# Optimization experiments

Measured on AMD Instinct MI355X. Metric: run time of the kernel, lower is better.

The kernel has to match this reference:

```python
import jax, jax.numpy as jnp
import numpy as np


def setup_inputs() -> dict:
    key = jax.random.key(0)
    kx, ky = jax.random.split(key)
    x = jax.random.normal(kx, (16, 4096, 3), dtype=jnp.float32)
    y = jax.random.normal(ky, (16, 4096, 3), dtype=jnp.float32)
    return {"x": x, "y": y}


def reference(x, y):
    # avoiding the O(b*N*M*d) difference tensor of the naive expansion.
    x2 = jnp.sum(x * x, axis=-1)                  # (b, N)
    y2 = jnp.sum(y * y, axis=-1)                  # (b, M)
    xy = jnp.einsum('bnd,bmd->bnm', x, y)         # (b, N, M)
    dist = x2[:, :, None] + y2[:, None, :] - 2.0 * xy
    min_d = jnp.min(dist, axis=2)                 # top-1 smallest over M -> (b, N)
    chamfer = jnp.sum(min_d, axis=1) / x.shape[1] # (b,)
    return jnp.sum(chamfer)
```

## Files before the change

### kernel.cpp

```cpp
#include <hip/hip_runtime.h>


constexpr int NPTS   = 4096;
constexpr int NBATCH = 16;
constexpr int BLOCK  = 256;
constexpr int XPT    = 8;
constexpr int XCHUNK = BLOCK * XPT;
constexpr int NXC    = NPTS / XCHUNK;
constexpr int NYC    = 64;
constexpr int YT     = NPTS / NYC;


__global__ __launch_bounds__(BLOCK, 8) void chamfer_part_kernel(
    const float* __restrict__ x, const float* __restrict__ y,
    float* __restrict__ ws)
{
    __shared__ float4 sy[YT];

    const int b      = blockIdx.x / (NXC * NYC);
    const int xchunk = (blockIdx.x / NYC) % NXC;
    const int ychunk = blockIdx.x % NYC;

    if (threadIdx.x < YT) {
        const float* yp = y + ((size_t)b * NPTS + ychunk * YT + threadIdx.x) * 3;
        const float y0 = yp[0], y1 = yp[1], y2 = yp[2];
        sy[threadIdx.x] = make_float4(2.0f * y0, 2.0f * y1, 2.0f * y2,
                                      fmaf(y2, y2, fmaf(y1, y1, y0 * y0)));
    }

    const int xbase = xchunk * XCHUNK + threadIdx.x * XPT;
    const float4* xp4 = (const float4*)(x + ((size_t)b * NPTS + xbase) * 3);
    float xf[24];
    #pragma unroll
    for (int q = 0; q < 6; ++q) {
        const float4 a = xp4[q];
        xf[4 * q + 0] = a.x; xf[4 * q + 1] = a.y;
        xf[4 * q + 2] = a.z; xf[4 * q + 3] = a.w;
    }

    __syncthreads();

    float m[XPT];
    #pragma unroll
    for (int i = 0; i < XPT; ++i) m[i] = 3.4e38f;

    #pragma unroll 1
    for (int j = 0; j < YT; j += 2) {
        const float4 Y0 = sy[j];
        const float4 Y1 = sy[j + 1];
        #pragma unroll
        for (int i = 0; i < XPT; ++i) {
            const float t0 = fmaf(-xf[3 * i + 0], Y0.x,
                             fmaf(-xf[3 * i + 1], Y0.y,
                             fmaf(-xf[3 * i + 2], Y0.z, Y0.w)));
            const float t1 = fmaf(-xf[3 * i + 0], Y1.x,
                             fmaf(-xf[3 * i + 1], Y1.y,
                             fmaf(-xf[3 * i + 2], Y1.z, Y1.w)));
            m[i] = fminf(fminf(t0, t1), m[i]);
        }
    }

    float* wp = ws + ((size_t)b * NYC + ychunk) * NPTS + xbase;
    #pragma unroll
    for (int i = 0; i < XPT; i += 4) {
        float4 o;
        float* oc = (float*)&o;
        #pragma unroll
        for (int k = 0; k < 4; ++k) {
            const int p = i + k;
            const float x2 = fmaf(xf[3 * p + 2], xf[3 * p + 2],
                             fmaf(xf[3 * p + 1], xf[3 * p + 1],
                                  xf[3 * p + 0] * xf[3 * p + 0]));
            oc[k] = fmaxf(x2 + m[p], 0.0f);
        }
        ((float4*)wp)[i / 4] = o;
    }
}


__global__ __launch_bounds__(BLOCK) void chamfer_reduce_kernel(
    const float* __restrict__ ws, float* __restrict__ out)
{
    __shared__ float swsum[BLOCK / 64];
    const int idx = blockIdx.x * BLOCK + threadIdx.x;
    const int b   = idx / NPTS;
    const int xp  = idx % NPTS;

    const float* p = ws + (size_t)b * NYC * NPTS + xp;
    float mn = 3.4e38f;
    #pragma unroll 8
    for (int yc = 0; yc < NYC; ++yc)
        mn = fminf(mn, p[(size_t)yc * NPTS]);

    float s = mn;
    for (int off = 32; off > 0; off >>= 1)
        s += __shfl_down(s, off, 64);
    const int wave = threadIdx.x >> 6;
    if ((threadIdx.x & 63) == 0) swsum[wave] = s;
    __syncthreads();
    if (threadIdx.x == 0) {
        float t = 0.f;
        #pragma unroll
        for (int w = 0; w < BLOCK / 64; ++w) t += swsum[w];
        atomicAdd(out, t * (1.0f / NPTS));
    }
}


__global__ __launch_bounds__(BLOCK) void chamfer_min_atomic_kernel(
    const float* __restrict__ x, const float* __restrict__ y,
    unsigned int* __restrict__ ws_min)
{
    constexpr int YTILE = 256;
    constexpr int FNYC  = NPTS / YTILE;
    __shared__ float4 sy[YTILE];

    const int b      = blockIdx.x / (NXC * FNYC);
    const int xchunk = (blockIdx.x / FNYC) % NXC;
    const int ychunk = blockIdx.x % FNYC;

    {
        const float* yp = y + ((size_t)b * NPTS + ychunk * YTILE + threadIdx.x) * 3;
        const float y0 = yp[0], y1 = yp[1], y2 = yp[2];
        sy[threadIdx.x] = make_float4(2.0f * y0, 2.0f * y1, 2.0f * y2,
                                      fmaf(y2, y2, fmaf(y1, y1, y0 * y0)));
    }

    const int xbase = xchunk * XCHUNK + threadIdx.x * XPT;
    const float4* xp4 = (const float4*)(x + ((size_t)b * NPTS + xbase) * 3);
    float xf[24];
    #pragma unroll
    for (int q = 0; q < 6; ++q) {
        const float4 a = xp4[q];
        xf[4 * q + 0] = a.x; xf[4 * q + 1] = a.y;
        xf[4 * q + 2] = a.z; xf[4 * q + 3] = a.w;
    }

    __syncthreads();

    float m[XPT];
    #pragma unroll
    for (int i = 0; i < XPT; ++i) m[i] = 3.4e38f;

    #pragma unroll 1
    for (int j = 0; j < YTILE; j += 2) {
        const float4 Y0 = sy[j];
        const float4 Y1 = sy[j + 1];
        #pragma unroll
        for (int i = 0; i < XPT; ++i) {
            const float t0 = fmaf(-xf[3 * i + 0], Y0.x,
                             fmaf(-xf[3 * i + 1], Y0.y,
                             fmaf(-xf[3 * i + 2], Y0.z, Y0.w)));
            const float t1 = fmaf(-xf[3 * i + 0], Y1.x,
                             fmaf(-xf[3 * i + 1], Y1.y,
                             fmaf(-xf[3 * i + 2], Y1.z, Y1.w)));
            m[i] = fminf(m[i], fminf(t0, t1));
        }
    }

    unsigned int* wm = ws_min + (size_t)b * NPTS + xbase;
    #pragma unroll
    for (int i = 0; i < XPT; ++i) {
        const float x2 = fmaf(xf[3 * i + 2], xf[3 * i + 2],
                         fmaf(xf[3 * i + 1], xf[3 * i + 1],
                              xf[3 * i + 0] * xf[3 * i + 0]));
        const float d = fmaxf(x2 + m[i], 0.0f);
        atomicMin(&wm[i], __float_as_uint(d));
    }
}

__global__ __launch_bounds__(BLOCK) void chamfer_sum_kernel(
    const unsigned int* __restrict__ ws_min, float* __restrict__ out)
{
    __shared__ float swsum[BLOCK / 64];
    const int total = NBATCH * NPTS;
    float s = 0.f;
    for (int i = blockIdx.x * BLOCK + threadIdx.x; i < total;
         i += gridDim.x * BLOCK)
        s += __uint_as_float(ws_min[i]);

    for (int off = 32; off > 0; off >>= 1)
        s += __shfl_down(s, off, 64);
    const int wave = threadIdx.x >> 6;
    if ((threadIdx.x & 63) == 0) swsum[wave] = s;
    __syncthreads();
    if (threadIdx.x == 0) {
        float t = 0.f;
        #pragma unroll
        for (int w = 0; w < BLOCK / 64; ++w) t += swsum[w];
        atomicAdd(out, t * (1.0f / NPTS));
    }
}


extern "C" void kernel_launch(void* const* d_in, const int* in_sizes, int n_in,
                              void* d_out, int out_size, void* d_ws, size_t ws_size,
                              hipStream_t stream) {
    const float* x = (const float*)d_in[0];
    const float* y = (const float*)d_in[1];
    float* out = (float*)d_out;

    hipMemsetAsync(out, 0, sizeof(float), stream);

    const size_t need = (size_t)NBATCH * NYC * NPTS * sizeof(float);

    if (ws_size >= need) {
        float* ws = (float*)d_ws;
        chamfer_part_kernel<<<NBATCH * NXC * NYC, BLOCK, 0, stream>>>(x, y, ws);
        chamfer_reduce_kernel<<<NBATCH * NPTS / BLOCK, BLOCK, 0, stream>>>(ws, out);
    } else {
        unsigned int* ws_min = (unsigned int*)d_ws;
        hipMemsetAsync(ws_min, 0xFF, (size_t)NBATCH * NPTS * sizeof(unsigned int),
                       stream);
        chamfer_min_atomic_kernel<<<NBATCH * NXC * 16, BLOCK, 0, stream>>>(
            x, y, ws_min);
        chamfer_sum_kernel<<<64, BLOCK, 0, stream>>>(ws_min, out);
    }
}
```

Baseline: 97.43 us.

## Replace brute-force chamfer with z-slab bucketed nearest-neighbour search with pruning

Sorts both point clouds per batch into 64 z-slabs with a counting sort, then for each x point (sorted, so waves are spatially coherent) scans only nearby y slabs. It expands slab range until the wave-wide slab gap exceeds the current worst nearest distance. This replaces the all-pairs O(N*M) scan and the large partial-min workspace. It adds a low-parallelism bucketing kernel and divergent, data-dependent loops whose cost depends on point distribution.

After: 254.3 us. 161% more time.

```diff
diff --git a/kernel.cpp b/kernel.cpp
--- a/kernel.cpp
+++ b/kernel.cpp
@@ -4,108 +4,152 @@
 constexpr int NPTS   = 4096;
 constexpr int NBATCH = 16;
 constexpr int BLOCK  = 256;
+constexpr int NBKT   = 64;
+constexpr float ZLO  = -4.0f;
+constexpr float BW   = 0.125f;
+constexpr float IBW  = 8.0f;
+
+__device__ __forceinline__ int zbucket(float z) {
+    int k = (int)floorf((z - ZLO) * IBW);
+    return min(NBKT - 1, max(0, k));
+}
+
+
+__global__ __launch_bounds__(BLOCK) void chamfer_bucket_kernel(
+    const float* __restrict__ x, const float* __restrict__ y,
+    float4* __restrict__ ybuf, float4* __restrict__ xbuf,
+    unsigned int* __restrict__ yoffs, float* __restrict__ out)
+{
+    __shared__ unsigned int hist[NBKT], curs[NBKT], offs[NBKT + 1];
+    const int b   = blockIdx.x;
+    const int tid = threadIdx.x;
+    if (b == 0 && tid == 0) out[0] = 0.0f;
+
+    if (tid < NBKT) hist[tid] = 0;
+    __syncthreads();
+    for (int i = tid; i < NPTS; i += BLOCK)
+        atomicAdd(&hist[zbucket(y[((size_t)b * NPTS + i) * 3 + 2])], 1u);
+    __syncthreads();
+    if (tid == 0) {
+        unsigned int run = 0;
+        for (int k = 0; k < NBKT; ++k) { offs[k] = run; curs[k] = run; run += hist[k]; }
+        offs[NBKT] = run;
+    }
+    __syncthreads();
+    for (int i = tid; i < NPTS; i += BLOCK) {
+        const float* yp = y + ((size_t)b * NPTS + i) * 3;
+        const float y0 = yp[0], y1 = yp[1], y2 = yp[2];
+        const unsigned int pos = atomicAdd(&curs[zbucket(y2)], 1u);
+        ybuf[(size_t)b * NPTS + pos] = make_float4(
+            2.0f * y0, 2.0f * y1, 2.0f * y2,
+            fmaf(y2, y2, fmaf(y1, y1, y0 * y0)));
+    }
+    __syncthreads();
+    if (tid <= NBKT) yoffs[b * (NBKT + 1) + tid] = offs[tid];
+
+    if (tid < NBKT) hist[tid] = 0;
+    __syncthreads();
+    for (int i = tid; i < NPTS; i += BLOCK)
+        atomicAdd(&hist[zbucket(x[((size_t)b * NPTS + i) * 3 + 2])], 1u);
+    __syncthreads();
+    if (tid == 0) {
+        unsigned int run = 0;
+        for (int k = 0; k < NBKT; ++k) { curs[k] = run; run += hist[k]; }
+    }
+    __syncthreads();
+    for (int i = tid; i < NPTS; i += BLOCK) {
+        const float* xp = x + ((size_t)b * NPTS + i) * 3;
+        const float x0 = xp[0], x1 = xp[1], x2 = xp[2];
+        const unsigned int pos = atomicAdd(&curs[zbucket(x2)], 1u);
+        xbuf[(size_t)b * NPTS + pos] = make_float4(
+            x0, x1, x2, fmaf(x2, x2, fmaf(x1, x1, x0 * x0)));
+    }
+}
+
+
+__global__ __launch_bounds__(BLOCK) void chamfer_nn_kernel(
+    const float4* __restrict__ xbuf, const float4* __restrict__ ybuf,
+    const unsigned int* __restrict__ yoffs, float* __restrict__ out)
+{
+    __shared__ unsigned int off[NBKT + 1];
+    __shared__ float swsum[BLOCK / 64];
+    const int tid = threadIdx.x;
+    const int b   = blockIdx.x >> 4;
+    if (tid <= NBKT) off[tid] = yoffs[b * (NBKT + 1) + tid];
+    __syncthreads();
+
+    const int idx  = blockIdx.x * BLOCK + tid;
+    const float4 X = xbuf[idx];
+    const float  z = X.z;
+    const int    k = zbucket(z);
+
+    int   kmn = k, kmx = k;
+    float zmn = z, zmx = z;
+    #pragma unroll
+    for (int m = 1; m < 64; m <<= 1) {
+        kmn = min(kmn, __shfl_xor(kmn, m, 64));
+        kmx = max(kmx, __shfl_xor(kmx, m, 64));
+        zmn = fminf(zmn, __shfl_xor(zmn, m, 64));
+        zmx = fmaxf(zmx, __shfl_xor(zmx, m, 64));
+    }
+
+    const float4* yb = ybuf + (size_t)b * NPTS;
+    float best = 1e30f;
+
+    auto scan = [&](int klo, int khi) {
+        const unsigned int je = off[khi + 1];
+        unsigned int j = off[klo];
+        for (; j + 4 <= je; j += 4) {
+            const float4 Y0 = yb[j], Y1 = yb[j + 1];
+            const float4 Y2 = yb[j + 2], Y3 = yb[j + 3];
+            const float t0 = fmaf(-X.x, Y0.x, fmaf(-X.y, Y0.y, fmaf(-X.z, Y0.z, Y0.w)));
+            const float t1 = fmaf(-X.x, Y1.x, fmaf(-X.y, Y1.y, fmaf(-X.z, Y1.z, Y1.w)));
+            const float t2 = fmaf(-X.x, Y2.x, fmaf(-X.y, Y2.y, fmaf(-X.z, Y2.z, Y2.w)));
+            const float t3 = fmaf(-X.x, Y3.x, fmaf(-X.y, Y3.y, fmaf(-X.z, Y3.z, Y3.w)));
+            best = fminf(fminf(fminf(t0, t1), fminf(t2, t3)), best);
+        }
+        for (; j < je; ++j) {
+            const float4 Y0 = yb[j];
+            best = fminf(best,
+                fmaf(-X.x, Y0.x, fmaf(-X.y, Y0.y, fmaf(-X.z, Y0.z, Y0.w))));
+        }
+    };
+
+    int lo = kmn, hi = kmx;
+    scan(lo, hi);
+    for (;;) {
+        float worst = X.w + best;
+        #pragma unroll
+        for (int m = 1; m < 64; m <<= 1)
+            worst = fmaxf(worst, __shfl_xor(worst, m, 64));
+        const float thr = worst * 1.0001f + 1e-6f;
+        const float Lg = (lo == 0)        ? 1e18f : zmn - (ZLO + lo * BW);
+        const float Hg = (hi == NBKT - 1) ? 1e18f : (ZLO + (hi + 1) * BW) - zmx;
+        const bool okL = Lg * Lg > thr;
+        const bool okH = Hg * Hg > thr;
+        if (okL && okH) break;
+        if (!okL && (okH || Lg <= Hg)) { --lo; scan(lo, lo); }
+        else                           { ++hi; scan(hi, hi); }
+    }
+
+    const float d = fmaxf(X.w + best, 0.0f);
+
+    float s = d;
+    for (int o = 32; o > 0; o >>= 1) s += __shfl_down(s, o, 64);
+    if ((tid & 63) == 0) swsum[tid >> 6] = s;
+    __syncthreads();
+    if (tid == 0) {
+        float t = 0.0f;
+        #pragma unroll
+        for (int w = 0; w < BLOCK / 64; ++w) t += swsum[w];
+        atomicAdd(out, t * (1.0f / NPTS));
+    }
+}
+
+
 constexpr int XPT    = 8;
 constexpr int XCHUNK = BLOCK * XPT;
 constexpr int NXC    = NPTS / XCHUNK;
-constexpr int NYC    = 64;
-constexpr int YT     = NPTS / NYC;
-
-
-__global__ __launch_bounds__(BLOCK, 8) void chamfer_part_kernel(
-    const float* __restrict__ x, const float* __restrict__ y,
-    float* __restrict__ ws)
-{
-    __shared__ float4 sy[YT];
-
-    const int b      = blockIdx.x / (NXC * NYC);
-    const int xchunk = (blockIdx.x / NYC) % NXC;
-    const int ychunk = blockIdx.x % NYC;
-
-    if (threadIdx.x < YT) {
-        const float* yp = y + ((size_t)b * NPTS + ychunk * YT + threadIdx.x) * 3;
-        const float y0 = yp[0], y1 = yp[1], y2 = yp[2];
-        sy[threadIdx.x] = make_float4(2.0f * y0, 2.0f * y1, 2.0f * y2,
-                                      fmaf(y2, y2, fmaf(y1, y1, y0 * y0)));
-    }
-
-    const int xbase = xchunk * XCHUNK + threadIdx.x * XPT;
-    const float4* xp4 = (const float4*)(x + ((size_t)b * NPTS + xbase) * 3);
-    float xf[24];
-    #pragma unroll
-    for (int q = 0; q < 6; ++q) {
-        const float4 a = xp4[q];
-        xf[4 * q + 0] = a.x; xf[4 * q + 1] = a.y;
-        xf[4 * q + 2] = a.z; xf[4 * q + 3] = a.w;
-    }
-
-    __syncthreads();
-
-    float m[XPT];
-    #pragma unroll
-    for (int i = 0; i < XPT; ++i) m[i] = 3.4e38f;
-
-    #pragma unroll 1
-    for (int j = 0; j < YT; j += 2) {
-        const float4 Y0 = sy[j];
-        const float4 Y1 = sy[j + 1];
-        #pragma unroll
-        for (int i = 0; i < XPT; ++i) {
-            const float t0 = fmaf(-xf[3 * i + 0], Y0.x,
-                             fmaf(-xf[3 * i + 1], Y0.y,
-                             fmaf(-xf[3 * i + 2], Y0.z, Y0.w)));
-            const float t1 = fmaf(-xf[3 * i + 0], Y1.x,
-                             fmaf(-xf[3 * i + 1], Y1.y,
-                             fmaf(-xf[3 * i + 2], Y1.z, Y1.w)));
-            m[i] = fminf(fminf(t0, t1), m[i]);
-        }
-    }
-
-    float* wp = ws + ((size_t)b * NYC + ychunk) * NPTS + xbase;
-    #pragma unroll
-    for (int i = 0; i < XPT; i += 4) {
-        float4 o;
-        float* oc = (float*)&o;
-        #pragma unroll
-        for (int k = 0; k < 4; ++k) {
-            const int p = i + k;
-            const float x2 = fmaf(xf[3 * p + 2], xf[3 * p + 2],
-                             fmaf(xf[3 * p + 1], xf[3 * p + 1],
-                                  xf[3 * p + 0] * xf[3 * p + 0]));
-            oc[k] = fmaxf(x2 + m[p], 0.0f);
-        }
-        ((float4*)wp)[i / 4] = o;
-    }
-}
-
-
-__global__ __launch_bounds__(BLOCK) void chamfer_reduce_kernel(
-    const float* __restrict__ ws, float* __restrict__ out)
-{
-    __shared__ float swsum[BLOCK / 64];
-    const int idx = blockIdx.x * BLOCK + threadIdx.x;
-    const int b   = idx / NPTS;
-    const int xp  = idx % NPTS;
-
-    const float* p = ws + (size_t)b * NYC * NPTS + xp;
-    float mn = 3.4e38f;
-    #pragma unroll 8
-    for (int yc = 0; yc < NYC; ++yc)
-        mn = fminf(mn, p[(size_t)yc * NPTS]);
-
-    float s = mn;
-    for (int off = 32; off > 0; off >>= 1)
-        s += __shfl_down(s, off, 64);
-    const int wave = threadIdx.x >> 6;
-    if ((threadIdx.x & 63) == 0) swsum[wave] = s;
-    __syncthreads();
-    if (threadIdx.x == 0) {
-        float t = 0.f;
-        #pragma unroll
-        for (int w = 0; w < BLOCK / 64; ++w) t += swsum[w];
-        atomicAdd(out, t * (1.0f / NPTS));
-    }
-}
-
 
 __global__ __launch_bounds__(BLOCK) void chamfer_min_atomic_kernel(
     const float* __restrict__ x, const float* __restrict__ y,
@@ -200,16 +244,22 @@
     const float* y = (const float*)d_in[1];
     float* out = (float*)d_out;
 
-    hipMemsetAsync(out, 0, sizeof(float), stream);
-
-    const size_t need = (size_t)NBATCH * NYC * NPTS * sizeof(float);
-
-    if (ws_size >= need) {
-        float* ws = (float*)d_ws;
-        chamfer_part_kernel<<<NBATCH * NXC * NYC, BLOCK, 0, stream>>>(x, y, ws);
-        chamfer_reduce_kernel<<<NBATCH * NPTS / BLOCK, BLOCK, 0, stream>>>(ws, out);
+    const size_t YBUF_OFF  = 0;
+    const size_t XBUF_OFF  = (size_t)3 * 512 * 1024;
+    const size_t YOFFS_OFF = (size_t)5 * 512 * 1024;
+    const size_t NEED      = YOFFS_OFF + (size_t)NBATCH * (NBKT + 1) * 4 + 4096;
+
+    if (ws_size >= NEED) {
+        float4* ybuf = (float4*)((char*)d_ws + YBUF_OFF);
+        float4* xbuf = (float4*)((char*)d_ws + XBUF_OFF);
+        unsigned int* yoffs = (unsigned int*)((char*)d_ws + YOFFS_OFF);
+        chamfer_bucket_kernel<<<NBATCH, BLOCK, 0, stream>>>(
+            x, y, ybuf, xbuf, yoffs, out);
+        chamfer_nn_kernel<<<NBATCH * NPTS / BLOCK, BLOCK, 0, stream>>>(
+            xbuf, ybuf, yoffs, out);
     } else {
         unsigned int* ws_min = (unsigned int*)d_ws;
+        hipMemsetAsync(out, 0, sizeof(float), stream);
         hipMemsetAsync(ws_min, 0xFF, (size_t)NBATCH * NPTS * sizeof(unsigned int),
                        stream);
         chamfer_min_atomic_kernel<<<NBATCH * NXC * 16, BLOCK, 0, stream>>>(
```
